# Kernel tuning notes

Measured on AMD Instinct MI355X. Metric: run time of the kernel, lower is better.

Reference implementation:

```python
import jax, jax.numpy as jnp
import numpy as np

DIM = 512
NUM_HEADS = 8
DIM_HEAD = 64
EPS = 1e-8
ROPE_THETA = 10000.0


def rms_norm(x, gamma):
    # F.normalize(x, dim=-1, p=2, eps) * sqrt(dim) * gamma
    norm = jnp.sqrt(jnp.sum(x * x, axis=-1, keepdims=True))
    x = x / jnp.maximum(norm, EPS)
    return x * (DIM ** 0.5) * gamma


def apply_rope(x):
    # x: [b, h, n, d], interleaved-pair RoPE (rotary-embedding-torch style)
    n, d = x.shape[-2], x.shape[-1]
    inv_freq = 1.0 / (ROPE_THETA ** (jnp.arange(0, d, 2, dtype=jnp.float32) / d))
    freqs = jnp.arange(n, dtype=jnp.float32)[:, None] * inv_freq[None, :]  # [n, d/2]
    freqs = jnp.repeat(freqs, 2, axis=-1)  # [n, d]
    cos, sin = jnp.cos(freqs), jnp.sin(freqs)
    x1 = x[..., ::2]
    x2 = x[..., 1::2]
    rot = jnp.stack((-x2, x1), axis=-1).reshape(x.shape)
    return x * cos + rot * sin


def setup_inputs() -> dict:
    key = jax.random.key(0)
    k1, k2, k3, k4 = jax.random.split(key, 4)
    b, n = 4, 2048
    dim_inner = NUM_HEADS * DIM_HEAD
    x = jax.random.normal(k1, (b, n, DIM), dtype=jnp.float32)
    gamma = jnp.ones((DIM,), dtype=jnp.float32)
    w_qkv = jax.random.normal(k2, (DIM, 3 * dim_inner), dtype=jnp.float32) * (DIM ** -0.5)
    w_out = jax.random.normal(k3, (dim_inner, DIM), dtype=jnp.float32) * (dim_inner ** -0.5)
    return {"x": x, "gamma": gamma, "w_qkv": w_qkv, "w_out": w_out}


def reference(x, gamma, w_qkv, w_out):
    b, n, _ = x.shape
    h, d = NUM_HEADS, DIM_HEAD
    xn = rms_norm(x, gamma)
    qkv = xn @ w_qkv  # [b, n, 3*h*d]
    qkv = qkv.reshape(b, n, 3, h, d)
    q = jnp.transpose(qkv[:, :, 0], (0, 2, 1, 3))  # [b, h, n, d]
    k = jnp.transpose(qkv[:, :, 1], (0, 2, 1, 3))
    v = jnp.transpose(qkv[:, :, 2], (0, 2, 1, 3))
    q = apply_rope(q)
    k = apply_rope(k)
    scale = d ** -0.5
    attn = jnp.einsum('bhnd,bhmd->bhnm', q, k) * scale
    attn = jax.nn.softmax(attn, axis=-1)
    out = jnp.einsum('bhnm,bhmd->bhnd', attn, v)
    out = jnp.transpose(out, (0, 2, 1, 3)).reshape(b, n, h * d)
    return out @ w_out
```

## Files before the change

### kernel.cpp

```cpp
#include <hip/hip_runtime.h>
#include <hip/hip_bf16.h>
#include <cmath>

#define B_SZ 4
#define N_SEQ 2048
#define DIM 512
#define NH 8
#define DH 64
#define QKV_N 1536
#define ROWS (B_SZ * N_SEQ)

typedef __bf16 bf16x8 __attribute__((ext_vector_type(8)));
typedef __bf16 bf16x4 __attribute__((ext_vector_type(4)));
typedef float  f32x4  __attribute__((ext_vector_type(4)));

#define GLOAD_LDS16(gp, lp)                                                     \
    __builtin_amdgcn_global_load_lds(                                           \
        (const __attribute__((address_space(1))) void*)(gp),                    \
        (__attribute__((address_space(3))) void*)(lp), 16, 0, 0)

#define MFMA_BF16 __builtin_amdgcn_mfma_f32_16x16x32_bf16

#define SBAR() asm volatile("s_barrier" ::: "memory")

__device__ __forceinline__ void tcast_tile(const float* __restrict__ W,
                                           __bf16* __restrict__ Wt,
                                           int K, int N, int n0, int k0, int t,
                                           float (*Ls)[68]) {
    const int tx = t & 15, ty = t >> 4;
    #pragma unroll
    for (int i = 0; i < 4; i++) {
        int k = ty + i * 16;
        float4 v = *(const float4*)&W[(size_t)(k0 + k) * N + n0 + tx * 4];
        *(float4*)&Ls[k][tx * 4] = v;
    }
    __syncthreads();
    const int nrow = t >> 2, seg = (t & 3) * 16;
    bf16x8 o0, o1;
    #pragma unroll
    for (int j = 0; j < 8; j++) o0[j] = (__bf16)Ls[seg + j][nrow];
    #pragma unroll
    for (int j = 0; j < 8; j++) o1[j] = (__bf16)Ls[seg + 8 + j][nrow];
    *(bf16x8*)&Wt[(size_t)(n0 + nrow) * K + k0 + seg]     = o0;
    *(bf16x8*)&Wt[(size_t)(n0 + nrow) * K + k0 + seg + 8] = o1;
}

__global__ __launch_bounds__(256) void prelude_kernel(const float* __restrict__ x,
                                                      const float* __restrict__ gamma,
                                                      const float* __restrict__ w_qkv,
                                                      const float* __restrict__ w_out,
                                                      __bf16* __restrict__ A,
                                                      __bf16* __restrict__ Wqkvt,
                                                      __bf16* __restrict__ Woutt) {
    __shared__ float Ls[64][68];
    const int bx = blockIdx.x, t = threadIdx.x;
    if (bx < 2048) {
        const int row  = bx * 4 + (t >> 6);
        const int lane = t & 63;
        const float4* xr = (const float4*)(x + (size_t)row * DIM);
        float4 a = xr[lane];
        float4 b = xr[lane + 64];
        float ss = a.x*a.x + a.y*a.y + a.z*a.z + a.w*a.w
                 + b.x*b.x + b.y*b.y + b.z*b.z + b.w*b.w;
        #pragma unroll
        for (int off = 32; off > 0; off >>= 1) ss += __shfl_xor(ss, off, 64);
        float s = 22.62741699796952f / fmaxf(sqrtf(ss), 1e-8f);
        const float4* gr = (const float4*)gamma;
        float4 g1 = gr[lane], g2 = gr[lane + 64];
        bf16x4 o1 = { (__bf16)(a.x*g1.x*s), (__bf16)(a.y*g1.y*s),
                      (__bf16)(a.z*g1.z*s), (__bf16)(a.w*g1.w*s) };
        bf16x4 o2 = { (__bf16)(b.x*g2.x*s), (__bf16)(b.y*g2.y*s),
                      (__bf16)(b.z*g2.z*s), (__bf16)(b.w*g2.w*s) };
        *(bf16x4*)(A + (size_t)row * DIM + lane * 4)       = o1;
        *(bf16x4*)(A + (size_t)row * DIM + 256 + lane * 4) = o2;
    } else {
        const int idx = bx - 2048;
        const int k0 = (idx >> 5) * 64, c = idx & 31;
        if (c < 24) tcast_tile(w_qkv, Wqkvt, DIM, QKV_N, c * 64, k0, t, Ls);
        else        tcast_tile(w_out, Woutt, DIM, DIM, (c - 24) * 64, k0, t, Ls);
    }
}

template <int N, typename OutT>
__global__ __launch_bounds__(256) void gemm_bf16_kernel(const __bf16* __restrict__ A,
                                                        const __bf16* __restrict__ Bt,
                                                        OutT* __restrict__ C) {
    __shared__ __bf16 As[2][128 * 32];
    __shared__ __bf16 Bs[2][128 * 32];
    const int t = threadIdx.x;
    const int lane = t & 63;
    const int w = t >> 6;
    const int l16 = lane & 15, quad = lane >> 4;
    const int wr = w >> 1, wc = w & 1;
    const int row0 = blockIdx.y * 128, col0 = blockIdx.x * 128;

    f32x4 acc[4][4] = {};

    const int r0a = t >> 2,         ks0 = (t & 3) * 8;
    const int r1a = (t + 256) >> 2;

    auto dma = [&](int kidx, int bb) {
        const int kt = kidx * 32;
        GLOAD_LDS16(A  + (size_t)(row0 + r0a) * DIM + kt + ks0, As[bb] + t * 8);
        GLOAD_LDS16(A  + (size_t)(row0 + r1a) * DIM + kt + ks0, As[bb] + (t + 256) * 8);
        GLOAD_LDS16(Bt + (size_t)(col0 + r0a) * DIM + kt + ks0, Bs[bb] + t * 8);
        GLOAD_LDS16(Bt + (size_t)(col0 + r1a) * DIM + kt + ks0, Bs[bb] + (t + 256) * 8);
    };

    dma(0, 0);
    for (int i = 0; i < 16; i++) {
        const int cur = i & 1;
        SBAR();
        if (i + 1 < 16) {
            dma(i + 1, cur ^ 1);
            asm volatile("s_waitcnt vmcnt(4)" ::: "memory");
        } else {
            asm volatile("s_waitcnt vmcnt(0)" ::: "memory");
        }
        SBAR();

        bf16x8 af[4], bfr[4];
        #pragma unroll
        for (int mi = 0; mi < 4; mi++)
            af[mi] = *(const bf16x8*)(As[cur] + (wr * 64 + mi * 16 + l16) * 32 + quad * 8);
        #pragma unroll
        for (int ni = 0; ni < 4; ni++)
            bfr[ni] = *(const bf16x8*)(Bs[cur] + (wc * 64 + ni * 16 + l16) * 32 + quad * 8);
        __builtin_amdgcn_s_setprio(1);
        #pragma unroll
        for (int mi = 0; mi < 4; mi++)
            #pragma unroll
            for (int ni = 0; ni < 4; ni++)
                acc[mi][ni] = MFMA_BF16(af[mi], bfr[ni], acc[mi][ni], 0, 0, 0);
        __builtin_amdgcn_s_setprio(0);
    }
    #pragma unroll
    for (int mi = 0; mi < 4; mi++) {
        #pragma unroll
        for (int ni = 0; ni < 4; ni++) {
            #pragma unroll
            for (int r = 0; r < 4; r++) {
                int m = row0 + wr * 64 + mi * 16 + quad * 4 + r;
                int n = col0 + wc * 64 + ni * 16 + l16;
                if constexpr (sizeof(OutT) == 4) {
                    C[(size_t)m * N + n] = acc[mi][ni][r];
                } else {
                    C[(size_t)m * N + n] = (__bf16)acc[mi][ni][r];
                }
            }
        }
    }
}

__global__ __launch_bounds__(256) void gemm_out_kernel(const __bf16* __restrict__ A,
                                                       const __bf16* __restrict__ Bt,
                                                       float* __restrict__ C) {
    __shared__ __bf16 As[2][64 * 32];
    __shared__ __bf16 Bs[2][128 * 32];
    const int t = threadIdx.x;
    const int lane = t & 63;
    const int w = t >> 6;
    const int l16 = lane & 15, quad = lane >> 4;
    const int wr = w >> 1, wc = w & 1;
    const int row0 = blockIdx.y * 64, col0 = blockIdx.x * 128;

    f32x4 acc[2][4] = {};

    const int r0a = t >> 2, ks0 = (t & 3) * 8;
    const int r1a = (t + 256) >> 2;

    auto dma = [&](int kidx, int bb) {
        const int kt = kidx * 32;
        GLOAD_LDS16(A  + (size_t)(row0 + r0a) * DIM + kt + ks0, As[bb] + t * 8);
        GLOAD_LDS16(Bt + (size_t)(col0 + r0a) * DIM + kt + ks0, Bs[bb] + t * 8);
        GLOAD_LDS16(Bt + (size_t)(col0 + r1a) * DIM + kt + ks0, Bs[bb] + (t + 256) * 8);
    };

    dma(0, 0);
    for (int i = 0; i < 16; i++) {
        const int cur = i & 1;
        SBAR();
        if (i + 1 < 16) {
            dma(i + 1, cur ^ 1);
            asm volatile("s_waitcnt vmcnt(3)" ::: "memory");
        } else {
            asm volatile("s_waitcnt vmcnt(0)" ::: "memory");
        }
        SBAR();

        bf16x8 af[2], bfr[4];
        #pragma unroll
        for (int mi = 0; mi < 2; mi++)
            af[mi] = *(const bf16x8*)(As[cur] + (wr * 32 + mi * 16 + l16) * 32 + quad * 8);
        #pragma unroll
        for (int ni = 0; ni < 4; ni++)
            bfr[ni] = *(const bf16x8*)(Bs[cur] + (wc * 64 + ni * 16 + l16) * 32 + quad * 8);
        __builtin_amdgcn_s_setprio(1);
        #pragma unroll
        for (int mi = 0; mi < 2; mi++)
            #pragma unroll
            for (int ni = 0; ni < 4; ni++)
                acc[mi][ni] = MFMA_BF16(af[mi], bfr[ni], acc[mi][ni], 0, 0, 0);
        __builtin_amdgcn_s_setprio(0);
    }
    #pragma unroll
    for (int mi = 0; mi < 2; mi++)
        #pragma unroll
        for (int ni = 0; ni < 4; ni++)
            #pragma unroll
            for (int r = 0; r < 4; r++) {
                int m = row0 + wr * 32 + mi * 16 + quad * 4 + r;
                int n = col0 + wc * 64 + ni * 16 + l16;
                C[(size_t)m * 512 + n] = acc[mi][ni][r];
            }
}

__global__ __launch_bounds__(256) void prep_kernel(const __bf16* __restrict__ qkvb,
                                                   __bf16* __restrict__ Qb,
                                                   __bf16* __restrict__ Kf,
                                                   __bf16* __restrict__ Vf) {
    const int bx = blockIdx.x;
    const int nt = bx & 31;
    const int bh = bx >> 5;
    const int b  = bh >> 3;
    const int h  = bh & 7;
    const int t  = threadIdx.x;
    const float QSCALE = 0.18033688011112042f;

    {
        const int r  = t >> 2;
        const int d0 = (t & 3) << 4;
        const int pos = nt * 64 + r;
        const __bf16* qp = qkvb + (size_t)(b * N_SEQ + pos) * QKV_N + h * DH + d0;

        union Pack { __bf16 h[16]; uint4 u[2]; };
        Pack qi, ki, qo, ko;
        qi.u[0] = ((const uint4*)qp)[0];         qi.u[1] = ((const uint4*)qp)[1];
        ki.u[0] = ((const uint4*)(qp + 512))[0]; ki.u[1] = ((const uint4*)(qp + 512))[1];

        #pragma unroll
        for (int i = 0; i < 8; i++) {
            int p = (d0 >> 1) + i;
            float inv = exp2f(-0.41524101186092028f * (float)p);
            float ang = (float)pos * inv;
            float sn, cs;
            sincosf(ang, &sn, &cs);
            float qe = (float)qi.h[2*i], qd = (float)qi.h[2*i+1];
            float ke = (float)ki.h[2*i], kd = (float)ki.h[2*i+1];
            qo.h[2*i]   = (__bf16)(QSCALE * (qe * cs - qd * sn));
            qo.h[2*i+1] = (__bf16)(QSCALE * (qd * cs + qe * sn));
            ko.h[2*i]   = (__bf16)(ke * cs - kd * sn);
            ko.h[2*i+1] = (__bf16)(kd * cs + ke * sn);
        }
        uint4* qd_ = (uint4*)(Qb + ((size_t)bh * N_SEQ + pos) * DH + d0);
        qd_[0] = qo.u[0]; qd_[1] = qo.u[1];
        const int group = r >> 4, kl = r & 15;
        const int c = d0 >> 5, quad = (d0 & 31) >> 3;
        __bf16* kdst = Kf + ((size_t)bh * 32 + nt) * 4096
                          + (group * 2 + c) * 512 + (quad * 16 + kl) * 8;
        *(uint4*)kdst         = ko.u[0];
        *(uint4*)(kdst + 128) = ko.u[1];
    }

    {
        const int w = t >> 6, lane = t & 63;
        union PackV { __bf16 h[16]; unsigned long long q[4]; };
        PackV v;
        #pragma unroll
        for (int j = 0; j < 16; j++) {
            int row = nt * 64 + w * 16 + j;
            v.h[j] = qkvb[(size_t)(b * N_SEQ + row) * QKV_N + 1024 + h * DH + lane];
        }
        const int ng = lane >> 4, vl = lane & 15;
        __bf16* vdst = Vf + ((size_t)bh * 32 + nt) * 4096
                          + (ng * 2 + (w >> 1)) * 512 + vl * 8 + (w & 1) * 4;
        #pragma unroll
        for (int q = 0; q < 4; q++)
            *(unsigned long long*)(vdst + q * 128) = v.q[q];
    }
}

__global__ __launch_bounds__(256, 2) void attn_mfma_kernel(const __bf16* __restrict__ Qb,
                                                           const __bf16* __restrict__ Kf,
                                                           const __bf16* __restrict__ Vf,
                                                           __bf16* __restrict__ attn) {
    __shared__ __bf16 kv[2][2][8192];

    const int t    = threadIdx.x;
    const int w    = t >> 6;
    const int lane = t & 63;
    const int l16  = lane & 15;
    const int quad = lane >> 4;
    const int qh   = w >> 1;
    const int kp   = w & 1;

    const int bx = blockIdx.x;
    const int bh = bx & 31;
    const int qc = bx >> 5;
    const int b  = bh >> 3;
    const int h  = bh & 7;

    const int qrow0 = qc * 128 + qh * 64;
    const __bf16* Qh = Qb + ((size_t)bh * N_SEQ + qrow0) * DH;
    const __bf16* Kt = Kf + (size_t)bh * 32 * 4096;
    const __bf16* Vt = Vf + (size_t)bh * 32 * 4096;

    bf16x8 qa[4][2];
    #pragma unroll
    for (int f = 0; f < 4; f++) {
        qa[f][0] = *(const bf16x8*)(Qh + (size_t)(f * 16 + l16) * DH + quad * 8);
        qa[f][1] = *(const bf16x8*)(Qh + (size_t)(f * 16 + l16) * DH + 32 + quad * 8);
    }

    bf16x8 ones;
    #pragma unroll
    for (int i = 0; i < 8; i++) ones[i] = (__bf16)1.0f;

    f32x4 O[4][4] = {};
    f32x4 L[4] = {};

    auto dma_tile = [&](int tidx, int p, int pp) {
        const __bf16* kss = Kt + (size_t)tidx * 4096;
        const __bf16* vss = Vt + (size_t)tidx * 4096;
        __bf16* dst = &kv[p][pp][0];
        GLOAD_LDS16(kss + t * 8,        dst + t * 8);
        GLOAD_LDS16(kss + 2048 + t * 8, dst + 2048 + t * 8);
        GLOAD_LDS16(vss + t * 8,        dst + 4096 + t * 8);
        GLOAD_LDS16(vss + 2048 + t * 8, dst + 4096 + 2048 + t * 8);
    };

    dma_tile(0, 0, 0);
    dma_tile(1, 1, 0);
    for (int i = 0; i < 16; i++) {
        const int cur = i & 1;
        SBAR();
        if (i + 1 < 16) {
            dma_tile(2 * (i + 1),     0, cur ^ 1);
            dma_tile(2 * (i + 1) + 1, 1, cur ^ 1);
            asm volatile("s_waitcnt vmcnt(8)" ::: "memory");
        } else {
            asm volatile("s_waitcnt vmcnt(0)" ::: "memory");
        }
        SBAR();

        const __bf16* kb = &kv[kp][cur][0];
        const __bf16* vb = &kv[kp][cur][4096];

        bf16x8 kf[4][2];
        #pragma unroll
        for (int g = 0; g < 4; g++)
            #pragma unroll
            for (int c = 0; c < 2; c++)
                kf[g][c] = *(const bf16x8*)(kb + (g * 2 + c) * 512 + lane * 8);

        bf16x8 pa[4][2];
        #pragma unroll
        for (int f = 0; f < 4; f++) {
            f32x4 S[4];
            __builtin_amdgcn_s_setprio(1);
            #pragma unroll
            for (int g = 0; g < 4; g++) {
                f32x4 z = {0, 0, 0, 0};
                z = MFMA_BF16(kf[g][0], qa[f][0], z, 0, 0, 0);
                z = MFMA_BF16(kf[g][1], qa[f][1], z, 0, 0, 0);
                S[g] = z;
            }
            __builtin_amdgcn_s_setprio(0);
            #pragma unroll
            for (int j = 0; j < 8; j++) {
                pa[f][0][j] = (__bf16)__builtin_amdgcn_exp2f(S[(j >> 2)][j & 3]);
                pa[f][1][j] = (__bf16)__builtin_amdgcn_exp2f(S[2 + (j >> 2)][j & 3]);
            }
        }

        bf16x8 vf[4][2];
        #pragma unroll
        for (int n = 0; n < 4; n++)
            #pragma unroll
            for (int kc = 0; kc < 2; kc++)
                vf[n][kc] = *(const bf16x8*)(vb + (n * 2 + kc) * 512 + lane * 8);

        __builtin_amdgcn_s_setprio(1);
        #pragma unroll
        for (int f = 0; f < 4; f++) {
            #pragma unroll
            for (int n = 0; n < 4; n++) {
                O[f][n] = MFMA_BF16(pa[f][0], vf[n][0], O[f][n], 0, 0, 0);
                O[f][n] = MFMA_BF16(pa[f][1], vf[n][1], O[f][n], 0, 0, 0);
            }
            L[f] = MFMA_BF16(pa[f][0], ones, L[f], 0, 0, 0);
            L[f] = MFMA_BF16(pa[f][1], ones, L[f], 0, 0, 0);
        }
        __builtin_amdgcn_s_setprio(0);
    }

    __syncthreads();
    float* reds = (float*)&kv[0][0][0];
    float* myO = reds + (size_t)(qh * 64 + lane) * 68;
    float* myL = reds + 128 * 68 + (size_t)(qh * 64 + lane) * 20;
    if (kp == 1) {
        #pragma unroll
        for (int f = 0; f < 4; f++) {
            #pragma unroll
            for (int n = 0; n < 4; n++)
                *(f32x4*)(myO + (f * 4 + n) * 4) = O[f][n];
            *(f32x4*)(myL + f * 4) = L[f];
        }
    }
    __syncthreads();
    if (kp == 0) {
        #pragma unroll
        for (int f = 0; f < 4; f++) {
            #pragma unroll
            for (int n = 0; n < 4; n++)
                O[f][n] += *(const f32x4*)(myO + (f * 4 + n) * 4);
            L[f] += *(const f32x4*)(myL + f * 4);
        }
        #pragma unroll
        for (int f = 0; f < 4; f++) {
            float inv[4];
            #pragma unroll
            for (int r = 0; r < 4; r++) inv[r] = 1.0f / L[f][r];
            #pragma unroll
            for (int n = 0; n < 4; n++)
                #pragma unroll
                for (int r = 0; r < 4; r++) {
                    size_t row = (size_t)(b * N_SEQ + qrow0 + f * 16 + quad * 4 + r);
                    attn[row * 512 + h * DH + n * 16 + l16] =
                        (__bf16)(O[f][n][r] * inv[r]);
                }
        }
    }
}

extern "C" void kernel_launch(void* const* d_in, const int* in_sizes, int n_in,
                              void* d_out, int out_size, void* d_ws, size_t ws_size,
                              hipStream_t stream) {
    const float* x     = (const float*)d_in[0];
    const float* gamma = (const float*)d_in[1];
    const float* w_qkv = (const float*)d_in[2];
    const float* w_out = (const float*)d_in[3];
    float* out = (float*)d_out;

    __bf16* Abf   = (__bf16*)d_ws;
    __bf16* Wqkvt = Abf + (size_t)ROWS * DIM;
    __bf16* Woutt = Wqkvt + (size_t)QKV_N * DIM;
    __bf16* qkvb  = Woutt + (size_t)DIM * DIM;
    __bf16* attnb = qkvb;
    __bf16* Qb    = qkvb + (size_t)ROWS * QKV_N;
    __bf16* Kf    = Qb + (size_t)NH * B_SZ * N_SEQ * DH;
    __bf16* Vf    = Kf + (size_t)NH * B_SZ * N_SEQ * DH;

    prelude_kernel<<<2304, 256, 0, stream>>>(x, gamma, w_qkv, w_out,
                                             Abf, Wqkvt, Woutt);
    gemm_bf16_kernel<QKV_N, __bf16><<<dim3(QKV_N / 128, ROWS / 128), 256, 0, stream>>>(
        Abf, Wqkvt, qkvb);
    prep_kernel<<<1024, 256, 0, stream>>>(qkvb, Qb, Kf, Vf);
    attn_mfma_kernel<<<512, 256, 0, stream>>>(Qb, Kf, Vf, attnb);
    gemm_out_kernel<<<dim3(4, 128), 256, 0, stream>>>(attnb, Woutt, out);
}
```

Baseline: 153.1 us.

## Fuse V fragment layout into QKV GEMM epilogue and triple-buffer GEMM loads

The QKV GEMM blocks that produce V columns now write V directly in the MFMA-fragment layout the attention kernel expects, so the prep kernel no longer rereads V from the qkv buffer and scatters it. Both GEMMs move from double- to triple-buffered LDS staging, issuing loads two K-steps ahead with adjusted vmcnt waits. This removes a strided V gather pass and gives more load/compute overlap, at the cost of more LDS per block and a more specialised epilogue.

```diff
diff --git a/kernel.cpp b/kernel.cpp
--- a/kernel.cpp
+++ b/kernel.cpp
@@ -81,12 +81,12 @@
     }
 }
 
-template <int N, typename OutT>
-__global__ __launch_bounds__(256) void gemm_bf16_kernel(const __bf16* __restrict__ A,
-                                                        const __bf16* __restrict__ Bt,
-                                                        OutT* __restrict__ C) {
-    __shared__ __bf16 As[2][128 * 32];
-    __shared__ __bf16 Bs[2][128 * 32];
+__global__ __launch_bounds__(256) void gemm_qkv_kernel(const __bf16* __restrict__ A,
+                                                       const __bf16* __restrict__ Bt,
+                                                       __bf16* __restrict__ C,
+                                                       __bf16* __restrict__ Vf) {
+    __shared__ __bf16 As[3][128 * 32];
+    __shared__ __bf16 Bs[3][128 * 32];
     const int t = threadIdx.x;
     const int lane = t & 63;
     const int w = t >> 6;
@@ -96,7 +96,7 @@
 
     f32x4 acc[4][4] = {};
 
-    const int r0a = t >> 2,         ks0 = (t & 3) * 8;
+    const int r0a = t >> 2, ks0 = (t & 3) * 8;
     const int r1a = (t + 256) >> 2;
 
     auto dma = [&](int kidx, int bb) {
@@ -108,11 +108,14 @@
     };
 
     dma(0, 0);
+    dma(1, 1);
+    int cb = 0, wb = 2;
     for (int i = 0; i < 16; i++) {
-        const int cur = i & 1;
-        SBAR();
-        if (i + 1 < 16) {
-            dma(i + 1, cur ^ 1);
+        SBAR();
+        if (i + 2 < 16) {
+            dma(i + 2, wb);
+            asm volatile("s_waitcnt vmcnt(8)" ::: "memory");
+        } else if (i + 1 < 16) {
             asm volatile("s_waitcnt vmcnt(4)" ::: "memory");
         } else {
             asm volatile("s_waitcnt vmcnt(0)" ::: "memory");
@@ -122,10 +125,10 @@
         bf16x8 af[4], bfr[4];
         #pragma unroll
         for (int mi = 0; mi < 4; mi++)
-            af[mi] = *(const bf16x8*)(As[cur] + (wr * 64 + mi * 16 + l16) * 32 + quad * 8);
+            af[mi] = *(const bf16x8*)(As[cb] + (wr * 64 + mi * 16 + l16) * 32 + quad * 8);
         #pragma unroll
         for (int ni = 0; ni < 4; ni++)
-            bfr[ni] = *(const bf16x8*)(Bs[cur] + (wc * 64 + ni * 16 + l16) * 32 + quad * 8);
+            bfr[ni] = *(const bf16x8*)(Bs[cb] + (wc * 64 + ni * 16 + l16) * 32 + quad * 8);
         __builtin_amdgcn_s_setprio(1);
         #pragma unroll
         for (int mi = 0; mi < 4; mi++)
@@ -133,30 +136,45 @@
             for (int ni = 0; ni < 4; ni++)
                 acc[mi][ni] = MFMA_BF16(af[mi], bfr[ni], acc[mi][ni], 0, 0, 0);
         __builtin_amdgcn_s_setprio(0);
-    }
-    #pragma unroll
-    for (int mi = 0; mi < 4; mi++) {
-        #pragma unroll
-        for (int ni = 0; ni < 4; ni++) {
-            #pragma unroll
-            for (int r = 0; r < 4; r++) {
-                int m = row0 + wr * 64 + mi * 16 + quad * 4 + r;
-                int n = col0 + wc * 64 + ni * 16 + l16;
-                if constexpr (sizeof(OutT) == 4) {
-                    C[(size_t)m * N + n] = acc[mi][ni][r];
-                } else {
-                    C[(size_t)m * N + n] = (__bf16)acc[mi][ni][r];
+        cb = (cb == 2) ? 0 : cb + 1;
+        wb = (wb == 2) ? 0 : wb + 1;
+    }
+
+    if (blockIdx.x >= 8) {
+        const int head  = (blockIdx.x - 8) * 2 + wc;
+        const int mbase = row0 + wr * 64;
+        const int b     = mbase >> 11;
+        const int nt    = (mbase >> 6) & 31;
+        __bf16* vt = Vf + ((size_t)(b * 8 + head) * 32 + nt) * 4096;
+        #pragma unroll
+        for (int ni = 0; ni < 4; ni++)
+            #pragma unroll
+            for (int kc = 0; kc < 2; kc++) {
+                bf16x8 o = { (__bf16)acc[2*kc][ni][0],   (__bf16)acc[2*kc][ni][1],
+                             (__bf16)acc[2*kc][ni][2],   (__bf16)acc[2*kc][ni][3],
+                             (__bf16)acc[2*kc+1][ni][0], (__bf16)acc[2*kc+1][ni][1],
+                             (__bf16)acc[2*kc+1][ni][2], (__bf16)acc[2*kc+1][ni][3] };
+                *(bf16x8*)(vt + (ni * 2 + kc) * 512 + lane * 8) = o;
+            }
+    } else {
+        #pragma unroll
+        for (int mi = 0; mi < 4; mi++)
+            #pragma unroll
+            for (int ni = 0; ni < 4; ni++)
+                #pragma unroll
+                for (int r = 0; r < 4; r++) {
+                    int m = row0 + wr * 64 + mi * 16 + quad * 4 + r;
+                    int n = col0 + wc * 64 + ni * 16 + l16;
+                    C[(size_t)m * QKV_N + n] = (__bf16)acc[mi][ni][r];
                 }
-            }
-        }
     }
 }
 
 __global__ __launch_bounds__(256) void gemm_out_kernel(const __bf16* __restrict__ A,
                                                        const __bf16* __restrict__ Bt,
                                                        float* __restrict__ C) {
-    __shared__ __bf16 As[2][64 * 32];
-    __shared__ __bf16 Bs[2][128 * 32];
+    __shared__ __bf16 As[3][64 * 32];
+    __shared__ __bf16 Bs[3][128 * 32];
     const int t = threadIdx.x;
     const int lane = t & 63;
     const int w = t >> 6;
@@ -177,11 +195,14 @@
     };
 
     dma(0, 0);
+    dma(1, 1);
+    int cb = 0, wb = 2;
     for (int i = 0; i < 16; i++) {
-        const int cur = i & 1;
-        SBAR();
-        if (i + 1 < 16) {
-            dma(i + 1, cur ^ 1);
+        SBAR();
+        if (i + 2 < 16) {
+            dma(i + 2, wb);
+            asm volatile("s_waitcnt vmcnt(6)" ::: "memory");
+        } else if (i + 1 < 16) {
             asm volatile("s_waitcnt vmcnt(3)" ::: "memory");
         } else {
             asm volatile("s_waitcnt vmcnt(0)" ::: "memory");
@@ -191,10 +212,10 @@
         bf16x8 af[2], bfr[4];
         #pragma unroll
         for (int mi = 0; mi < 2; mi++)
-            af[mi] = *(const bf16x8*)(As[cur] + (wr * 32 + mi * 16 + l16) * 32 + quad * 8);
+            af[mi] = *(const bf16x8*)(As[cb] + (wr * 32 + mi * 16 + l16) * 32 + quad * 8);
         #pragma unroll
         for (int ni = 0; ni < 4; ni++)
-            bfr[ni] = *(const bf16x8*)(Bs[cur] + (wc * 64 + ni * 16 + l16) * 32 + quad * 8);
+            bfr[ni] = *(const bf16x8*)(Bs[cb] + (wc * 64 + ni * 16 + l16) * 32 + quad * 8);
         __builtin_amdgcn_s_setprio(1);
         #pragma unroll
         for (int mi = 0; mi < 2; mi++)
@@ -202,6 +223,8 @@
             for (int ni = 0; ni < 4; ni++)
                 acc[mi][ni] = MFMA_BF16(af[mi], bfr[ni], acc[mi][ni], 0, 0, 0);
         __builtin_amdgcn_s_setprio(0);
+        cb = (cb == 2) ? 0 : cb + 1;
+        wb = (wb == 2) ? 0 : wb + 1;
     }
     #pragma unroll
     for (int mi = 0; mi < 2; mi++)
@@ -217,8 +240,7 @@
 
 __global__ __launch_bounds__(256) void prep_kernel(const __bf16* __restrict__ qkvb,
                                                    __bf16* __restrict__ Qb,
-                                                   __bf16* __restrict__ Kf,
-                                                   __bf16* __restrict__ Vf) {
+                                                   __bf16* __restrict__ Kf) {
     const int bx = blockIdx.x;
     const int nt = bx & 31;
     const int bh = bx >> 5;
@@ -227,57 +249,38 @@
     const int t  = threadIdx.x;
     const float QSCALE = 0.18033688011112042f;
 
-    {
-        const int r  = t >> 2;
-        const int d0 = (t & 3) << 4;
-        const int pos = nt * 64 + r;
-        const __bf16* qp = qkvb + (size_t)(b * N_SEQ + pos) * QKV_N + h * DH + d0;
-
-        union Pack { __bf16 h[16]; uint4 u[2]; };
-        Pack qi, ki, qo, ko;
-        qi.u[0] = ((const uint4*)qp)[0];         qi.u[1] = ((const uint4*)qp)[1];
-        ki.u[0] = ((const uint4*)(qp + 512))[0]; ki.u[1] = ((const uint4*)(qp + 512))[1];
-
-        #pragma unroll
-        for (int i = 0; i < 8; i++) {
-            int p = (d0 >> 1) + i;
-            float inv = exp2f(-0.41524101186092028f * (float)p);
-            float ang = (float)pos * inv;
-            float sn, cs;
-            sincosf(ang, &sn, &cs);
-            float qe = (float)qi.h[2*i], qd = (float)qi.h[2*i+1];
-            float ke = (float)ki.h[2*i], kd = (float)ki.h[2*i+1];
-            qo.h[2*i]   = (__bf16)(QSCALE * (qe * cs - qd * sn));
-            qo.h[2*i+1] = (__bf16)(QSCALE * (qd * cs + qe * sn));
-            ko.h[2*i]   = (__bf16)(ke * cs - kd * sn);
-            ko.h[2*i+1] = (__bf16)(kd * cs + ke * sn);
-        }
-        uint4* qd_ = (uint4*)(Qb + ((size_t)bh * N_SEQ + pos) * DH + d0);
-        qd_[0] = qo.u[0]; qd_[1] = qo.u[1];
-        const int group = r >> 4, kl = r & 15;
-        const int c = d0 >> 5, quad = (d0 & 31) >> 3;
-        __bf16* kdst = Kf + ((size_t)bh * 32 + nt) * 4096
-                          + (group * 2 + c) * 512 + (quad * 16 + kl) * 8;
-        *(uint4*)kdst         = ko.u[0];
-        *(uint4*)(kdst + 128) = ko.u[1];
-    }
-
-    {
-        const int w = t >> 6, lane = t & 63;
-        union PackV { __bf16 h[16]; unsigned long long q[4]; };
-        PackV v;
-        #pragma unroll
-        for (int j = 0; j < 16; j++) {
-            int row = nt * 64 + w * 16 + j;
-            v.h[j] = qkvb[(size_t)(b * N_SEQ + row) * QKV_N + 1024 + h * DH + lane];
-        }
-        const int ng = lane >> 4, vl = lane & 15;
-        __bf16* vdst = Vf + ((size_t)bh * 32 + nt) * 4096
-                          + (ng * 2 + (w >> 1)) * 512 + vl * 8 + (w & 1) * 4;
-        #pragma unroll
-        for (int q = 0; q < 4; q++)
-            *(unsigned long long*)(vdst + q * 128) = v.q[q];
-    }
+    const int r  = t >> 2;
+    const int d0 = (t & 3) << 4;
+    const int pos = nt * 64 + r;
+    const __bf16* qp = qkvb + (size_t)(b * N_SEQ + pos) * QKV_N + h * DH + d0;
+
+    union Pack { __bf16 h[16]; uint4 u[2]; };
+    Pack qi, ki, qo, ko;
+    qi.u[0] = ((const uint4*)qp)[0];         qi.u[1] = ((const uint4*)qp)[1];
+    ki.u[0] = ((const uint4*)(qp + 512))[0]; ki.u[1] = ((const uint4*)(qp + 512))[1];
+
+    #pragma unroll
+    for (int i = 0; i < 8; i++) {
+        int p = (d0 >> 1) + i;
+        float inv = exp2f(-0.41524101186092028f * (float)p);
+        float ang = (float)pos * inv;
+        float sn, cs;
+        sincosf(ang, &sn, &cs);
+        float qe = (float)qi.h[2*i], qd = (float)qi.h[2*i+1];
+        float ke = (float)ki.h[2*i], kd = (float)ki.h[2*i+1];
+        qo.h[2*i]   = (__bf16)(QSCALE * (qe * cs - qd * sn));
+        qo.h[2*i+1] = (__bf16)(QSCALE * (qd * cs + qe * sn));
+        ko.h[2*i]   = (__bf16)(ke * cs - kd * sn);
+        ko.h[2*i+1] = (__bf16)(kd * cs + ke * sn);
+    }
+    uint4* qd_ = (uint4*)(Qb + ((size_t)bh * N_SEQ + pos) * DH + d0);
+    qd_[0] = qo.u[0]; qd_[1] = qo.u[1];
+    const int group = r >> 4, kl = r & 15;
+    const int c = d0 >> 5, quad = (d0 & 31) >> 3;
+    __bf16* kdst = Kf + ((size_t)bh * 32 + nt) * 4096
+                      + (group * 2 + c) * 512 + (quad * 16 + kl) * 8;
+    *(uint4*)kdst         = ko.u[0];
+    *(uint4*)(kdst + 128) = ko.u[1];
 }
 
 __global__ __launch_bounds__(256, 2) void attn_mfma_kernel(const __bf16* __restrict__ Qb,
@@ -453,9 +456,9 @@
 
     prelude_kernel<<<2304, 256, 0, stream>>>(x, gamma, w_qkv, w_out,
                                              Abf, Wqkvt, Woutt);
-    gemm_bf16_kernel<QKV_N, __bf16><<<dim3(QKV_N / 128, ROWS / 128), 256, 0, stream>>>(
-        Abf, Wqkvt, qkvb);
-    prep_kernel<<<1024, 256, 0, stream>>>(qkvb, Qb, Kf, Vf);
+    gemm_qkv_kernel<<<dim3(QKV_N / 128, ROWS / 128), 256, 0, stream>>>(
+        Abf, Wqkvt, qkvb, Vf);
+    prep_kernel<<<1024, 256, 0, stream>>>(qkvb, Qb, Kf);
     attn_mfma_kernel<<<512, 256, 0, stream>>>(Qb, Kf, Vf, attnb);
     gemm_out_kernel<<<dim3(4, 128), 256, 0, stream>>>(attnb, Woutt, out);
 }
```

Measured after the change: 152.0 us. About the same (-0.8%).
